# Performance work log

Hardware: AMD Instinct MI355X
Metric: run time of the kernel (lower is better)

Reference implementation:

```python
import jax, jax.numpy as jnp
import numpy as np

B, L, LATENT, HID, NTOK = 65536, 8, 256, 128, 5


def setup_inputs() -> dict:
    key = jax.random.key(0)
    ks = jax.random.split(key, 8)
    s = 0.05  # small init scale for stable GRU dynamics
    return {
        "latent_context": jax.random.normal(ks[0], (B, LATENT), jnp.float32),
        "target_sequence": jax.random.randint(ks[1], (B, L), 0, NTOK),
        "emb_table": jax.random.normal(ks[2], (NTOK + 1, HID), jnp.float32) * s,
        "W_ih": jax.random.normal(ks[3], (3 * LATENT, HID), jnp.float32) * s,
        "W_hh": jax.random.normal(ks[4], (3 * LATENT, LATENT), jnp.float32) * s,
        "b_ih": jnp.zeros((3 * LATENT,), jnp.float32),
        "b_hh": jnp.zeros((3 * LATENT,), jnp.float32),
        "W_out": jax.random.normal(ks[5], (NTOK, LATENT), jnp.float32) * s,
        "b_out": jnp.zeros((NTOK,), jnp.float32),
    }


def reference(latent_context, target_sequence, emb_table, W_ih, W_hh, b_ih, b_hh, W_out, b_out):
    b = latent_context.shape[0]
    start_idx = emb_table.shape[0] - 1  # start token index = num_tokens
    # Teacher forcing: input token at step 0 is <start>, then target[:, :-1]
    tokens = jnp.concatenate(
        [jnp.full((b, 1), start_idx, dtype=target_sequence.dtype), target_sequence[:, :-1]],
        axis=1,
    )  # (B, L)
    emb = emb_table[tokens]  # (B, L, HID) embedding gather, done once

    def gru_step(h, x):
        # x: (B, HID), h: (B, LATENT). PyTorch GRU cell math.
        gi = x @ W_ih.T + b_ih          # (B, 3*LATENT)
        gh = h @ W_hh.T + b_hh          # (B, 3*LATENT)
        i_r, i_z, i_n = jnp.split(gi, 3, axis=-1)
        h_r, h_z, h_n = jnp.split(gh, 3, axis=-1)
        r = jax.nn.sigmoid(i_r + h_r)
        z = jax.nn.sigmoid(i_z + h_z)
        n = jnp.tanh(i_n + r * h_n)
        h_new = (1.0 - z) * n + z * h
        step_logits = h_new @ W_out.T + b_out  # (B, NTOK)
        return h_new, step_logits

    _, logits = jax.lax.scan(gru_step, latent_context, jnp.swapaxes(emb, 0, 1))
    return jnp.swapaxes(logits, 0, 1)  # (B, L, NTOK)
```

## Files before the change

### kernel.cpp

```cpp
#include <hip/hip_runtime.h>
#include <hip/hip_bf16.h>


typedef __attribute__((ext_vector_type(8)))  __bf16 bf16x8;
typedef __attribute__((ext_vector_type(4)))  __bf16 bf16x4;
typedef __attribute__((ext_vector_type(16))) float  f32x16;

__device__ __forceinline__ float sigm(float x) {
    return __builtin_amdgcn_rcpf(1.f + __expf(-x));
}
__device__ __forceinline__ float tanh_fast(float x) {
    return __builtin_fmaf(2.f, __builtin_amdgcn_rcpf(1.f + __expf(-2.f * x)), -1.f);
}
__device__ __forceinline__ float f4get(const float4& v, int i) {
    return i == 0 ? v.x : i == 1 ? v.y : i == 2 ? v.z : v.w;
}

__global__ void k_gtable(const float* __restrict__ emb, const float* __restrict__ W_ih,
                         const float* __restrict__ b_ih, const float* __restrict__ b_hh,
                         float* __restrict__ G) {
    int tok = blockIdx.x;
    int j   = threadIdx.x;
    const float4* e4 = (const float4*)(emb + tok * 128);
    const float4* w4 = (const float4*)(W_ih + (size_t)j * 128);
    float s = 0.f;
#pragma unroll
    for (int k = 0; k < 32; ++k) {
        float4 a = e4[k], b = w4[k];
        s += a.x * b.x + a.y * b.y + a.z * b.z + a.w * b.w;
    }
    s += b_ih[j];
    if (j < 512) s += b_hh[j];
    G[tok * 768 + j] = s;
}

__global__ void k_wfrag(const float* __restrict__ Whh, __bf16* __restrict__ Wg) {
    int u = blockIdx.x * 256 + threadIdx.x;
    int lane = u & 63;
    int kc   = (u >> 6) & 15;
    int w    = (u >> 10) & 7;
    int g    = u >> 13;
    int row  = g * 256 + w * 32 + (lane & 31);
    int k0   = kc * 16 + (lane >> 5) * 8;
    const float* src = Whh + (size_t)row * 256 + k0;
    bf16x8 v;
#pragma unroll
    for (int j = 0; j < 8; ++j) v[j] = (__bf16)src[j];
    *(bf16x8*)(Wg + (size_t)u * 8) = v;
}

__global__ __launch_bounds__(512, 2) void k_main(
    const float* __restrict__ latent, const int* __restrict__ tgt,
    const float* __restrict__ Gtab, const __bf16* __restrict__ Wg,
    const float* __restrict__ b_hh, const float* __restrict__ Wout,
    const float* __restrict__ bout, float* __restrict__ out) {

    __shared__ __bf16 h_lds[2][2][16][64][8];
    __shared__ __bf16 woutf_lds[16][64][8];
    __shared__ int    tok_lds[64 * 9];
    __shared__ float  gtab_lds[6 * 772];
    __shared__ float  bhn_lds[256];
    __shared__ float  logit_lds[64 * 40];

    const int tid  = threadIdx.x;
    const int lane = tid & 63;
    const int w    = tid >> 6;
    const int hk   = lane >> 5;
    const int bn   = lane & 31;
    const int row0 = blockIdx.x * 64;

    const __bf16* wa = Wg + (size_t)w * 8192 + (size_t)lane * 8;

    {
        int b = tid >> 3, t = tid & 7;
        tok_lds[b * 9 + t] = (t == 0) ? 5 : tgt[(size_t)(row0 + b) * 8 + t - 1];
    }
    if (tid < 256) bhn_lds[tid] = b_hh[512 + tid];
#pragma unroll
    for (int tok = 0; tok < 6; ++tok)
        for (int i = tid; i < 768; i += 512) gtab_lds[tok * 772 + i] = Gtab[tok * 768 + i];
    for (int kc = w; kc < 16; kc += 8) {
        bf16x8 v;
        if (bn < 5) {
            const float* src = Wout + bn * 256 + kc * 16 + hk * 8;
#pragma unroll
            for (int j = 0; j < 8; ++j) v[j] = (__bf16)src[j];
        } else {
#pragma unroll
            for (int j = 0; j < 8; ++j) v[j] = (__bf16)0.f;
        }
        *(bf16x8*)&woutf_lds[kc][lane][0] = v;
    }
    const float bo0 = bout[0], bo1 = bout[1], bo2 = bout[2], bo3 = bout[3], bo4 = bout[4];

#pragma unroll
    for (int nt = 0; nt < 2; ++nt) {
        int grow = row0 + nt * 32 + bn;
#pragma unroll
        for (int q = 0; q < 4; ++q) {
            int cb = w * 32 + q * 8 + hk * 4;
            float4 hv = *(const float4*)(latent + (size_t)grow * 256 + cb);
            bf16x4 hb;
            hb[0] = (__bf16)hv.x; hb[1] = (__bf16)hv.y;
            hb[2] = (__bf16)hv.z; hb[3] = (__bf16)hv.w;
            *(bf16x4*)&h_lds[0][nt][2 * w + (q >> 1)][(q & 1) * 32 + bn][4 * hk] = hb;
        }
    }
    __syncthreads();

    for (int t = 0; t < 8; ++t) {
        const int cur = t & 1, nxt = cur ^ 1;
        f32x16 acc[3][2];
        {
            f32x16 zz;
#pragma unroll
            for (int i = 0; i < 16; ++i) zz[i] = 0.f;
#pragma unroll
            for (int g = 0; g < 3; ++g)
#pragma unroll
                for (int nt = 0; nt < 2; ++nt) acc[g][nt] = zz;
        }
#pragma unroll 4
        for (int kc = 0; kc < 16; ++kc) {
            bf16x8 a0 = *(const bf16x8*)(wa + kc * 512);
            bf16x8 a1 = *(const bf16x8*)(wa + 65536 + kc * 512);
            bf16x8 a2 = *(const bf16x8*)(wa + 131072 + kc * 512);
            bf16x8 b0 = *(const bf16x8*)&h_lds[cur][0][kc][lane][0];
            bf16x8 b1 = *(const bf16x8*)&h_lds[cur][1][kc][lane][0];
            acc[0][0] = __builtin_amdgcn_mfma_f32_32x32x16_bf16(a0, b0, acc[0][0], 0, 0, 0);
            acc[0][1] = __builtin_amdgcn_mfma_f32_32x32x16_bf16(a0, b1, acc[0][1], 0, 0, 0);
            acc[1][0] = __builtin_amdgcn_mfma_f32_32x32x16_bf16(a1, b0, acc[1][0], 0, 0, 0);
            acc[1][1] = __builtin_amdgcn_mfma_f32_32x32x16_bf16(a1, b1, acc[1][1], 0, 0, 0);
            acc[2][0] = __builtin_amdgcn_mfma_f32_32x32x16_bf16(a2, b0, acc[2][0], 0, 0, 0);
            acc[2][1] = __builtin_amdgcn_mfma_f32_32x32x16_bf16(a2, b1, acc[2][1], 0, 0, 0);
        }

        if ((w == 0 || w == 7) && t > 0) {
            const int nt = (w == 0) ? 0 : 1;
            f32x16 lacc;
#pragma unroll
            for (int i = 0; i < 16; ++i) lacc[i] = 0.f;
#pragma unroll 4
            for (int kc = 0; kc < 16; ++kc) {
                bf16x8 wf = *(const bf16x8*)&woutf_lds[kc][lane][0];
                bf16x8 bb = *(const bf16x8*)&h_lds[cur][nt][kc][lane][0];
                lacc = __builtin_amdgcn_mfma_f32_32x32x16_bf16(wf, bb, lacc, 0, 0, 0);
            }
            float* dst = &logit_lds[(nt * 32 + bn) * 40 + (t - 1) * 5];
            if (hk == 0) {
                dst[0] = lacc[0] + bo0; dst[1] = lacc[1] + bo1;
                dst[2] = lacc[2] + bo2; dst[3] = lacc[3] + bo3;
            } else {
                dst[4] = lacc[0] + bo4;
            }
        }

#pragma unroll
        for (int nt = 0; nt < 2; ++nt) {
            int tok = tok_lds[(nt * 32 + bn) * 9 + t];
            const float* Gt = gtab_lds + tok * 772;
#pragma unroll
            for (int q = 0; q < 4; ++q) {
                int cb = w * 32 + q * 8 + hk * 4;
                float4 g0 = *(const float4*)(Gt + cb);
                float4 g1 = *(const float4*)(Gt + 256 + cb);
                float4 g2 = *(const float4*)(Gt + 512 + cb);
                float4 bh = *(const float4*)&bhn_lds[cb];
                bf16x4 hold = *(const bf16x4*)&h_lds[cur][nt][2 * w + (q >> 1)][(q & 1) * 32 + bn][4 * hk];
                bf16x4 hb;
#pragma unroll
                for (int i = 0; i < 4; ++i) {
                    int r = 4 * q + i;
                    float ar = acc[0][nt][r] + f4get(g0, i);
                    float az = acc[1][nt][r] + f4get(g1, i);
                    float hn = acc[2][nt][r] + f4get(bh, i);
                    float rg = sigm(ar);
                    float zg = sigm(az);
                    float ng = tanh_fast(__builtin_fmaf(rg, hn, f4get(g2, i)));
                    float hvv = ng + zg * ((float)hold[i] - ng);
                    hb[i] = (__bf16)hvv;
                }
                *(bf16x4*)&h_lds[nxt][nt][2 * w + (q >> 1)][(q & 1) * 32 + bn][4 * hk] = hb;
            }
        }
        __syncthreads();
    }

    if (w == 0 || w == 7) {
        const int nt = (w == 0) ? 0 : 1;
        f32x16 lacc;
#pragma unroll
        for (int i = 0; i < 16; ++i) lacc[i] = 0.f;
#pragma unroll 4
        for (int kc = 0; kc < 16; ++kc) {
            bf16x8 wf = *(const bf16x8*)&woutf_lds[kc][lane][0];
            bf16x8 bb = *(const bf16x8*)&h_lds[0][nt][kc][lane][0];
            lacc = __builtin_amdgcn_mfma_f32_32x32x16_bf16(wf, bb, lacc, 0, 0, 0);
        }
        float* dst = &logit_lds[(nt * 32 + bn) * 40 + 7 * 5];
        if (hk == 0) {
            dst[0] = lacc[0] + bo0; dst[1] = lacc[1] + bo1;
            dst[2] = lacc[2] + bo2; dst[3] = lacc[3] + bo3;
        } else {
            dst[4] = lacc[0] + bo4;
        }
    }
    __syncthreads();
    for (int i = tid; i < 64 * 40; i += 512)
        out[(size_t)row0 * 40 + i] = logit_lds[i];
}

extern "C" void kernel_launch(void* const* d_in, const int* in_sizes, int n_in,
                              void* d_out, int out_size, void* d_ws, size_t ws_size,
                              hipStream_t stream) {
    const float* latent = (const float*)d_in[0];
    const int*   tgt    = (const int*)d_in[1];
    const float* emb    = (const float*)d_in[2];
    const float* W_ih   = (const float*)d_in[3];
    const float* W_hh   = (const float*)d_in[4];
    const float* b_ih   = (const float*)d_in[5];
    const float* b_hh   = (const float*)d_in[6];
    const float* W_out  = (const float*)d_in[7];
    const float* b_out  = (const float*)d_in[8];
    float* out = (float*)d_out;

    float*  Gtab = (float*)d_ws;
    __bf16* Wg   = (__bf16*)((char*)d_ws + 18432);

    k_gtable<<<6, 768, 0, stream>>>(emb, W_ih, b_ih, b_hh, Gtab);
    k_wfrag<<<96, 256, 0, stream>>>(W_hh, Wg);
    k_main<<<1024, 512, 0, stream>>>(latent, tgt, Gtab, Wg, b_hh, W_out, b_out, out);
}
```

Measured before the change: 298.5 us.

## Fold token gate table into MFMA via one-hot operands and prefetch weight fragments

The per-token input-gate contributions and the b_hn bias are packed as an extra K=16 fragment per gate. They are applied by multiplying one-hot token vectors through MFMA, which removes the gather of gate values from LDS and the scalar adds in the gate epilogue. A fourth accumulator holds the input n-gate term separately. The first two K-chunks of the W_hh fragments are kept in registers and reloaded across the step to hide global or L2 latency. __syncthreads is replaced by a raw barrier with an explicit lgkmcnt wait. This adds 8 extra MFMAs per step and more register pressure, and it also rounds the gate table to bf16.

```diff
diff --git a/kernel.cpp b/kernel.cpp
--- a/kernel.cpp
+++ b/kernel.cpp
@@ -12,8 +12,11 @@
 __device__ __forceinline__ float tanh_fast(float x) {
     return __builtin_fmaf(2.f, __builtin_amdgcn_rcpf(1.f + __expf(-2.f * x)), -1.f);
 }
-__device__ __forceinline__ float f4get(const float4& v, int i) {
-    return i == 0 ? v.x : i == 1 ? v.y : i == 2 ? v.z : v.w;
+__device__ __forceinline__ void lds_barrier() {
+    __builtin_amdgcn_sched_barrier(0);
+    asm volatile("s_waitcnt lgkmcnt(0)" ::: "memory");
+    __builtin_amdgcn_s_barrier();
+    __builtin_amdgcn_sched_barrier(0);
 }
 
 __global__ void k_gtable(const float* __restrict__ emb, const float* __restrict__ W_ih,
@@ -34,32 +37,49 @@
     G[tok * 768 + j] = s;
 }
 
-__global__ void k_wfrag(const float* __restrict__ Whh, __bf16* __restrict__ Wg) {
-    int u = blockIdx.x * 256 + threadIdx.x;
+__global__ void k_wfrag2(const float* __restrict__ Whh, const float* __restrict__ Gtab,
+                         const float* __restrict__ b_hh, __bf16* __restrict__ Wg) {
+    int u    = blockIdx.x * 256 + threadIdx.x;
     int lane = u & 63;
-    int kc   = (u >> 6) & 15;
-    int w    = (u >> 10) & 7;
-    int g    = u >> 13;
-    int row  = g * 256 + w * 32 + (lane & 31);
-    int k0   = kc * 16 + (lane >> 5) * 8;
-    const float* src = Whh + (size_t)row * 256 + k0;
+    int frag = u >> 6;
+    int w    = frag / 52;
+    int f    = frag - 52 * w;
+    int m    = w * 32 + (lane & 31);
+    int cb   = (lane >> 5) * 8;
     bf16x8 v;
-#pragma unroll
-    for (int j = 0; j < 8; ++j) v[j] = (__bf16)src[j];
+    if (f == 51) {
+#pragma unroll
+        for (int j = 0; j < 8; ++j) {
+            int c = cb + j;
+            v[j] = (c < 6) ? (__bf16)Gtab[c * 768 + 512 + m] : (__bf16)0.f;
+        }
+    } else {
+        int g = f / 17, kc = f - 17 * g;
+        if (kc < 16) {
+            const float* src = Whh + (size_t)(g * 256 + m) * 256 + kc * 16 + cb;
+#pragma unroll
+            for (int j = 0; j < 8; ++j) v[j] = (__bf16)src[j];
+        } else {
+#pragma unroll
+            for (int j = 0; j < 8; ++j) {
+                int c = cb + j;
+                float val = 0.f;
+                if (c < 6) val = (g < 2) ? Gtab[c * 768 + g * 256 + m] : b_hh[512 + m];
+                v[j] = (__bf16)val;
+            }
+        }
+    }
     *(bf16x8*)(Wg + (size_t)u * 8) = v;
 }
 
 __global__ __launch_bounds__(512, 2) void k_main(
     const float* __restrict__ latent, const int* __restrict__ tgt,
-    const float* __restrict__ Gtab, const __bf16* __restrict__ Wg,
-    const float* __restrict__ b_hh, const float* __restrict__ Wout,
+    const __bf16* __restrict__ Wg, const float* __restrict__ Wout,
     const float* __restrict__ bout, float* __restrict__ out) {
 
     __shared__ __bf16 h_lds[2][2][16][64][8];
+    __shared__ __bf16 onehot_lds[8][2][64][8];
     __shared__ __bf16 woutf_lds[16][64][8];
-    __shared__ int    tok_lds[64 * 9];
-    __shared__ float  gtab_lds[6 * 772];
-    __shared__ float  bhn_lds[256];
     __shared__ float  logit_lds[64 * 40];
 
     const int tid  = threadIdx.x;
@@ -69,16 +89,29 @@
     const int bn   = lane & 31;
     const int row0 = blockIdx.x * 64;
 
-    const __bf16* wa = Wg + (size_t)w * 8192 + (size_t)lane * 8;
-
-    {
-        int b = tid >> 3, t = tid & 7;
-        tok_lds[b * 9 + t] = (t == 0) ? 5 : tgt[(size_t)(row0 + b) * 8 + t - 1];
-    }
-    if (tid < 256) bhn_lds[tid] = b_hh[512 + tid];
-#pragma unroll
-    for (int tok = 0; tok < 6; ++tok)
-        for (int i = tid; i < 768; i += 512) gtab_lds[tok * 772 + i] = Gtab[tok * 768 + i];
+    const __bf16* wbase = Wg + ((size_t)(w * 52) * 64 + lane) * 8;
+
+    bf16x8 A16_0 = *(const bf16x8*)(wbase + 16 * 512);
+    bf16x8 A16_1 = *(const bf16x8*)(wbase + 33 * 512);
+    bf16x8 A16_2 = *(const bf16x8*)(wbase + 50 * 512);
+    bf16x8 A16_3 = *(const bf16x8*)(wbase + 51 * 512);
+    bf16x8 p0a = *(const bf16x8*)(wbase + 0 * 512);
+    bf16x8 p0b = *(const bf16x8*)(wbase + 17 * 512);
+    bf16x8 p0c = *(const bf16x8*)(wbase + 34 * 512);
+    bf16x8 p1a = *(const bf16x8*)(wbase + 1 * 512);
+    bf16x8 p1b = *(const bf16x8*)(wbase + 18 * 512);
+    bf16x8 p1c = *(const bf16x8*)(wbase + 35 * 512);
+
+    for (int r = tid; r < 1024; r += 512) {
+        int t = r >> 7, nt = (r >> 6) & 1, ln = r & 63;
+        int brow = row0 + nt * 32 + (ln & 31);
+        int tok = (t == 0) ? 5 : tgt[(size_t)brow * 8 + t - 1];
+        int cbase = (ln >> 5) * 8;
+        bf16x8 v;
+#pragma unroll
+        for (int j = 0; j < 8; ++j) v[j] = (__bf16)((cbase + j == tok) ? 1.f : 0.f);
+        *(bf16x8*)&onehot_lds[t][nt][ln][0] = v;
+    }
     for (int kc = w; kc < 16; kc += 8) {
         bf16x8 v;
         if (bn < 5) {
@@ -110,21 +143,51 @@
 
     for (int t = 0; t < 8; ++t) {
         const int cur = t & 1, nxt = cur ^ 1;
-        f32x16 acc[3][2];
+        f32x16 acc[4][2];
         {
             f32x16 zz;
 #pragma unroll
             for (int i = 0; i < 16; ++i) zz[i] = 0.f;
 #pragma unroll
-            for (int g = 0; g < 3; ++g)
+            for (int g = 0; g < 4; ++g)
 #pragma unroll
                 for (int nt = 0; nt < 2; ++nt) acc[g][nt] = zz;
         }
-#pragma unroll 4
-        for (int kc = 0; kc < 16; ++kc) {
-            bf16x8 a0 = *(const bf16x8*)(wa + kc * 512);
-            bf16x8 a1 = *(const bf16x8*)(wa + 65536 + kc * 512);
-            bf16x8 a2 = *(const bf16x8*)(wa + 131072 + kc * 512);
+        {
+            bf16x8 oh0 = *(const bf16x8*)&onehot_lds[t][0][lane][0];
+            bf16x8 oh1 = *(const bf16x8*)&onehot_lds[t][1][lane][0];
+            acc[0][0] = __builtin_amdgcn_mfma_f32_32x32x16_bf16(A16_0, oh0, acc[0][0], 0, 0, 0);
+            acc[0][1] = __builtin_amdgcn_mfma_f32_32x32x16_bf16(A16_0, oh1, acc[0][1], 0, 0, 0);
+            acc[1][0] = __builtin_amdgcn_mfma_f32_32x32x16_bf16(A16_1, oh0, acc[1][0], 0, 0, 0);
+            acc[1][1] = __builtin_amdgcn_mfma_f32_32x32x16_bf16(A16_1, oh1, acc[1][1], 0, 0, 0);
+            acc[2][0] = __builtin_amdgcn_mfma_f32_32x32x16_bf16(A16_2, oh0, acc[2][0], 0, 0, 0);
+            acc[2][1] = __builtin_amdgcn_mfma_f32_32x32x16_bf16(A16_2, oh1, acc[2][1], 0, 0, 0);
+            acc[3][0] = __builtin_amdgcn_mfma_f32_32x32x16_bf16(A16_3, oh0, acc[3][0], 0, 0, 0);
+            acc[3][1] = __builtin_amdgcn_mfma_f32_32x32x16_bf16(A16_3, oh1, acc[3][1], 0, 0, 0);
+        }
+        {
+            bf16x8 b0 = *(const bf16x8*)&h_lds[cur][0][0][lane][0];
+            bf16x8 b1 = *(const bf16x8*)&h_lds[cur][1][0][lane][0];
+            acc[0][0] = __builtin_amdgcn_mfma_f32_32x32x16_bf16(p0a, b0, acc[0][0], 0, 0, 0);
+            acc[0][1] = __builtin_amdgcn_mfma_f32_32x32x16_bf16(p0a, b1, acc[0][1], 0, 0, 0);
+            acc[1][0] = __builtin_amdgcn_mfma_f32_32x32x16_bf16(p0b, b0, acc[1][0], 0, 0, 0);
+            acc[1][1] = __builtin_amdgcn_mfma_f32_32x32x16_bf16(p0b, b1, acc[1][1], 0, 0, 0);
+            acc[2][0] = __builtin_amdgcn_mfma_f32_32x32x16_bf16(p0c, b0, acc[2][0], 0, 0, 0);
+            acc[2][1] = __builtin_amdgcn_mfma_f32_32x32x16_bf16(p0c, b1, acc[2][1], 0, 0, 0);
+            b0 = *(const bf16x8*)&h_lds[cur][0][1][lane][0];
+            b1 = *(const bf16x8*)&h_lds[cur][1][1][lane][0];
+            acc[0][0] = __builtin_amdgcn_mfma_f32_32x32x16_bf16(p1a, b0, acc[0][0], 0, 0, 0);
+            acc[0][1] = __builtin_amdgcn_mfma_f32_32x32x16_bf16(p1a, b1, acc[0][1], 0, 0, 0);
+            acc[1][0] = __builtin_amdgcn_mfma_f32_32x32x16_bf16(p1b, b0, acc[1][0], 0, 0, 0);
+            acc[1][1] = __builtin_amdgcn_mfma_f32_32x32x16_bf16(p1b, b1, acc[1][1], 0, 0, 0);
+            acc[2][0] = __builtin_amdgcn_mfma_f32_32x32x16_bf16(p1c, b0, acc[2][0], 0, 0, 0);
+            acc[2][1] = __builtin_amdgcn_mfma_f32_32x32x16_bf16(p1c, b1, acc[2][1], 0, 0, 0);
+        }
+#pragma unroll 2
+        for (int kc = 2; kc < 16; ++kc) {
+            bf16x8 a0 = *(const bf16x8*)(wbase + kc * 512);
+            bf16x8 a1 = *(const bf16x8*)(wbase + (17 + kc) * 512);
+            bf16x8 a2 = *(const bf16x8*)(wbase + (34 + kc) * 512);
             bf16x8 b0 = *(const bf16x8*)&h_lds[cur][0][kc][lane][0];
             bf16x8 b1 = *(const bf16x8*)&h_lds[cur][1][kc][lane][0];
             acc[0][0] = __builtin_amdgcn_mfma_f32_32x32x16_bf16(a0, b0, acc[0][0], 0, 0, 0);
@@ -134,6 +197,12 @@
             acc[2][0] = __builtin_amdgcn_mfma_f32_32x32x16_bf16(a2, b0, acc[2][0], 0, 0, 0);
             acc[2][1] = __builtin_amdgcn_mfma_f32_32x32x16_bf16(a2, b1, acc[2][1], 0, 0, 0);
         }
+        p0a = *(const bf16x8*)(wbase + 0 * 512);
+        p0b = *(const bf16x8*)(wbase + 17 * 512);
+        p0c = *(const bf16x8*)(wbase + 34 * 512);
+        p1a = *(const bf16x8*)(wbase + 1 * 512);
+        p1b = *(const bf16x8*)(wbase + 18 * 512);
+        p1c = *(const bf16x8*)(wbase + 35 * 512);
 
         if ((w == 0 || w == 7) && t > 0) {
             const int nt = (w == 0) ? 0 : 1;
@@ -157,33 +226,23 @@
 
 #pragma unroll
         for (int nt = 0; nt < 2; ++nt) {
-            int tok = tok_lds[(nt * 32 + bn) * 9 + t];
-            const float* Gt = gtab_lds + tok * 772;
 #pragma unroll
             for (int q = 0; q < 4; ++q) {
-                int cb = w * 32 + q * 8 + hk * 4;
-                float4 g0 = *(const float4*)(Gt + cb);
-                float4 g1 = *(const float4*)(Gt + 256 + cb);
-                float4 g2 = *(const float4*)(Gt + 512 + cb);
-                float4 bh = *(const float4*)&bhn_lds[cb];
                 bf16x4 hold = *(const bf16x4*)&h_lds[cur][nt][2 * w + (q >> 1)][(q & 1) * 32 + bn][4 * hk];
                 bf16x4 hb;
 #pragma unroll
                 for (int i = 0; i < 4; ++i) {
                     int r = 4 * q + i;
-                    float ar = acc[0][nt][r] + f4get(g0, i);
-                    float az = acc[1][nt][r] + f4get(g1, i);
-                    float hn = acc[2][nt][r] + f4get(bh, i);
-                    float rg = sigm(ar);
-                    float zg = sigm(az);
-                    float ng = tanh_fast(__builtin_fmaf(rg, hn, f4get(g2, i)));
-                    float hvv = ng + zg * ((float)hold[i] - ng);
-                    hb[i] = (__bf16)hvv;
+                    float rg = sigm(acc[0][nt][r]);
+                    float zg = sigm(acc[1][nt][r]);
+                    float ng = tanh_fast(__builtin_fmaf(rg, acc[2][nt][r], acc[3][nt][r]));
+                    float hv = ng + zg * ((float)hold[i] - ng);
+                    hb[i] = (__bf16)hv;
                 }
                 *(bf16x4*)&h_lds[nxt][nt][2 * w + (q >> 1)][(q & 1) * 32 + bn][4 * hk] = hb;
             }
         }
-        __syncthreads();
+        lds_barrier();
     }
 
     if (w == 0 || w == 7) {
@@ -225,9 +284,9 @@
     float* out = (float*)d_out;
 
     float*  Gtab = (float*)d_ws;
-    __bf16* Wg   = (__bf16*)((char*)d_ws + 18432);
+    __bf16* Wg2  = (__bf16*)((char*)d_ws + 18432);
 
     k_gtable<<<6, 768, 0, stream>>>(emb, W_ih, b_ih, b_hh, Gtab);
-    k_wfrag<<<96, 256, 0, stream>>>(W_hh, Wg);
-    k_main<<<1024, 512, 0, stream>>>(latent, tgt, Gtab, Wg, b_hh, W_out, b_out, out);
-}
+    k_wfrag2<<<104, 256, 0, stream>>>(W_hh, Gtab, b_hh, Wg2);
+    k_main<<<1024, 512, 0, stream>>>(latent, tgt, Wg2, W_out, b_out, out);
+}
```

Result: faster. 288.8 us (-3.3%).

## Fold token gate table into MFMA via one-hot and switch to 16x16x32 tiles

Applied to the files above, without the earlier changes.

Replaces the per-element gather of the precomputed input-gate table and the b_hh_n bias with an extra MFMA k-chunk that multiplies the weights by a one-hot token matrix held in LDS. This removes the gate-table and token LDS lookups from the elementwise stage and adds a fourth accumulator group so the n-gate input term stays separate. The main kernel moves to 16x16x32 bf16 MFMA with 16 waves (1024 threads) per block and a lighter LDS-only barrier, which changes per-wave register pressure and occupancy. The gate table and bias are now rounded to bf16 inside the MFMA, which adds some precision loss.

```diff
diff --git a/kernel.cpp b/kernel.cpp
--- a/kernel.cpp
+++ b/kernel.cpp
@@ -4,7 +4,7 @@
 
 typedef __attribute__((ext_vector_type(8)))  __bf16 bf16x8;
 typedef __attribute__((ext_vector_type(4)))  __bf16 bf16x4;
-typedef __attribute__((ext_vector_type(16))) float  f32x16;
+typedef __attribute__((ext_vector_type(4)))  float  f32x4;
 
 __device__ __forceinline__ float sigm(float x) {
     return __builtin_amdgcn_rcpf(1.f + __expf(-x));
@@ -12,8 +12,11 @@
 __device__ __forceinline__ float tanh_fast(float x) {
     return __builtin_fmaf(2.f, __builtin_amdgcn_rcpf(1.f + __expf(-2.f * x)), -1.f);
 }
-__device__ __forceinline__ float f4get(const float4& v, int i) {
-    return i == 0 ? v.x : i == 1 ? v.y : i == 2 ? v.z : v.w;
+__device__ __forceinline__ void lds_barrier() {
+    __builtin_amdgcn_sched_barrier(0);
+    asm volatile("s_waitcnt lgkmcnt(0)" ::: "memory");
+    __builtin_amdgcn_s_barrier();
+    __builtin_amdgcn_sched_barrier(0);
 }
 
 __global__ void k_gtable(const float* __restrict__ emb, const float* __restrict__ W_ih,
@@ -34,179 +37,185 @@
     G[tok * 768 + j] = s;
 }
 
-__global__ void k_wfrag(const float* __restrict__ Whh, __bf16* __restrict__ Wg) {
-    int u = blockIdx.x * 256 + threadIdx.x;
+__global__ void k_wfrag3(const float* __restrict__ Whh, const float* __restrict__ Gtab,
+                         const float* __restrict__ b_hh, __bf16* __restrict__ Wg) {
+    int u    = blockIdx.x * 256 + threadIdx.x;
     int lane = u & 63;
-    int kc   = (u >> 6) & 15;
-    int w    = (u >> 10) & 7;
-    int g    = u >> 13;
-    int row  = g * 256 + w * 32 + (lane & 31);
-    int k0   = kc * 16 + (lane >> 5) * 8;
-    const float* src = Whh + (size_t)row * 256 + k0;
+    int frag = u >> 6;
+    int w    = frag / 28;
+    int f    = frag - 28 * w;
+    int col  = w * 16 + (lane & 15);
+    int kq   = lane >> 4;
     bf16x8 v;
-#pragma unroll
-    for (int j = 0; j < 8; ++j) v[j] = (__bf16)src[j];
+    if (f < 24) {
+        int g = f >> 3, kc = f & 7;
+        const float* src = Whh + (size_t)(g * 256 + col) * 256 + kc * 32 + kq * 8;
+#pragma unroll
+        for (int j = 0; j < 8; ++j) v[j] = (__bf16)src[j];
+    } else {
+        int g = f - 24;
+#pragma unroll
+        for (int j = 0; j < 8; ++j) {
+            int k = kq * 8 + j;
+            float val = 0.f;
+            if (k < 6) {
+                val = (g == 0) ? Gtab[k * 768 + col]
+                    : (g == 1) ? Gtab[k * 768 + 256 + col]
+                    : (g == 2) ? b_hh[512 + col]
+                               : Gtab[k * 768 + 512 + col];
+            }
+            v[j] = (__bf16)val;
+        }
+    }
     *(bf16x8*)(Wg + (size_t)u * 8) = v;
 }
 
-__global__ __launch_bounds__(512, 2) void k_main(
+__global__ __launch_bounds__(1024) void k_main(
     const float* __restrict__ latent, const int* __restrict__ tgt,
-    const float* __restrict__ Gtab, const __bf16* __restrict__ Wg,
-    const float* __restrict__ b_hh, const float* __restrict__ Wout,
+    const __bf16* __restrict__ Wg, const float* __restrict__ Wout,
     const float* __restrict__ bout, float* __restrict__ out) {
 
-    __shared__ __bf16 h_lds[2][2][16][64][8];
-    __shared__ __bf16 woutf_lds[16][64][8];
-    __shared__ int    tok_lds[64 * 9];
-    __shared__ float  gtab_lds[6 * 772];
-    __shared__ float  bhn_lds[256];
+    __shared__ __bf16 h_lds[2][4][8][64][8];
+    __shared__ __bf16 onehot_lds[8][4][64][8];
+    __shared__ __bf16 woutf_lds[8][64][8];
     __shared__ float  logit_lds[64 * 40];
 
     const int tid  = threadIdx.x;
     const int lane = tid & 63;
     const int w    = tid >> 6;
-    const int hk   = lane >> 5;
-    const int bn   = lane & 31;
+    const int q    = lane >> 4;
+    const int n16  = lane & 15;
     const int row0 = blockIdx.x * 64;
 
-    const __bf16* wa = Wg + (size_t)w * 8192 + (size_t)lane * 8;
-
-    {
-        int b = tid >> 3, t = tid & 7;
-        tok_lds[b * 9 + t] = (t == 0) ? 5 : tgt[(size_t)(row0 + b) * 8 + t - 1];
-    }
-    if (tid < 256) bhn_lds[tid] = b_hh[512 + tid];
-#pragma unroll
-    for (int tok = 0; tok < 6; ++tok)
-        for (int i = tid; i < 768; i += 512) gtab_lds[tok * 772 + i] = Gtab[tok * 768 + i];
-    for (int kc = w; kc < 16; kc += 8) {
+    const __bf16* wbase = Wg + ((size_t)(w * 28) * 64 + lane) * 8;
+
+    const int kc_h  = w >> 1;
+    const int slotl = n16 + 16 * ((2 * w + (q >> 1)) & 3);
+    const int joff  = 4 * (q & 1);
+
+    if (tid < 512) {
+        int kc = tid >> 6, ln = tid & 63, m = ln & 15, kq2 = ln >> 4;
         bf16x8 v;
-        if (bn < 5) {
-            const float* src = Wout + bn * 256 + kc * 16 + hk * 8;
-#pragma unroll
-            for (int j = 0; j < 8; ++j) v[j] = (__bf16)src[j];
-        } else {
-#pragma unroll
-            for (int j = 0; j < 8; ++j) v[j] = (__bf16)0.f;
-        }
-        *(bf16x8*)&woutf_lds[kc][lane][0] = v;
-    }
+#pragma unroll
+        for (int j = 0; j < 8; ++j)
+            v[j] = (m < 5) ? (__bf16)Wout[m * 256 + kc * 32 + kq2 * 8 + j] : (__bf16)0.f;
+        *(bf16x8*)&woutf_lds[kc][ln][0] = v;
+    }
+    for (int s = tid; s < 2048; s += 1024) {
+        int t = s >> 8, nt = (s >> 6) & 3, ln = s & 63;
+        int nn = ln & 15, kq2 = ln >> 4;
+        int tok = (t == 0) ? 5 : tgt[(size_t)(row0 + nt * 16 + nn) * 8 + t - 1];
+        bf16x8 v;
+#pragma unroll
+        for (int j = 0; j < 8; ++j) v[j] = (__bf16)((kq2 * 8 + j == tok) ? 1.f : 0.f);
+        *(bf16x8*)&onehot_lds[t][nt][ln][0] = v;
+    }
+#pragma unroll
+    for (int nt = 0; nt < 4; ++nt) {
+        float4 hv = *(const float4*)(latent + (size_t)(row0 + nt * 16 + n16) * 256 + 16 * w + 4 * q);
+        bf16x4 hb;
+        hb[0] = (__bf16)hv.x; hb[1] = (__bf16)hv.y;
+        hb[2] = (__bf16)hv.z; hb[3] = (__bf16)hv.w;
+        *(bf16x4*)&h_lds[0][nt][kc_h][slotl][joff] = hb;
+    }
+    const int lw = (w == 0) ? 0 : (w == 5) ? 1 : (w == 10) ? 2 : (w == 15) ? 3 : -1;
     const float bo0 = bout[0], bo1 = bout[1], bo2 = bout[2], bo3 = bout[3], bo4 = bout[4];
-
-#pragma unroll
-    for (int nt = 0; nt < 2; ++nt) {
-        int grow = row0 + nt * 32 + bn;
-#pragma unroll
-        for (int q = 0; q < 4; ++q) {
-            int cb = w * 32 + q * 8 + hk * 4;
-            float4 hv = *(const float4*)(latent + (size_t)grow * 256 + cb);
-            bf16x4 hb;
-            hb[0] = (__bf16)hv.x; hb[1] = (__bf16)hv.y;
-            hb[2] = (__bf16)hv.z; hb[3] = (__bf16)hv.w;
-            *(bf16x4*)&h_lds[0][nt][2 * w + (q >> 1)][(q & 1) * 32 + bn][4 * hk] = hb;
-        }
-    }
     __syncthreads();
 
     for (int t = 0; t < 8; ++t) {
         const int cur = t & 1, nxt = cur ^ 1;
-        f32x16 acc[3][2];
+        f32x4 acc[4][4];
+#pragma unroll
+        for (int g = 0; g < 4; ++g)
+#pragma unroll
+            for (int nt = 0; nt < 4; ++nt)
+#pragma unroll
+                for (int i = 0; i < 4; ++i) acc[g][nt][i] = 0.f;
+
+#pragma unroll 2
+        for (int kc = 0; kc < 8; ++kc) {
+            bf16x8 a0 = *(const bf16x8*)(wbase + (size_t)kc * 512);
+            bf16x8 a1 = *(const bf16x8*)(wbase + (size_t)(8 + kc) * 512);
+            bf16x8 a2 = *(const bf16x8*)(wbase + (size_t)(16 + kc) * 512);
+#pragma unroll
+            for (int nt = 0; nt < 4; ++nt) {
+                bf16x8 bb = *(const bf16x8*)&h_lds[cur][nt][kc][lane][0];
+                acc[0][nt] = __builtin_amdgcn_mfma_f32_16x16x32_bf16(a0, bb, acc[0][nt], 0, 0, 0);
+                acc[1][nt] = __builtin_amdgcn_mfma_f32_16x16x32_bf16(a1, bb, acc[1][nt], 0, 0, 0);
+                acc[2][nt] = __builtin_amdgcn_mfma_f32_16x16x32_bf16(a2, bb, acc[2][nt], 0, 0, 0);
+            }
+        }
         {
-            f32x16 zz;
-#pragma unroll
-            for (int i = 0; i < 16; ++i) zz[i] = 0.f;
-#pragma unroll
-            for (int g = 0; g < 3; ++g)
-#pragma unroll
-                for (int nt = 0; nt < 2; ++nt) acc[g][nt] = zz;
-        }
-#pragma unroll 4
-        for (int kc = 0; kc < 16; ++kc) {
-            bf16x8 a0 = *(const bf16x8*)(wa + kc * 512);
-            bf16x8 a1 = *(const bf16x8*)(wa + 65536 + kc * 512);
-            bf16x8 a2 = *(const bf16x8*)(wa + 131072 + kc * 512);
-            bf16x8 b0 = *(const bf16x8*)&h_lds[cur][0][kc][lane][0];
-            bf16x8 b1 = *(const bf16x8*)&h_lds[cur][1][kc][lane][0];
-            acc[0][0] = __builtin_amdgcn_mfma_f32_32x32x16_bf16(a0, b0, acc[0][0], 0, 0, 0);
-            acc[0][1] = __builtin_amdgcn_mfma_f32_32x32x16_bf16(a0, b1, acc[0][1], 0, 0, 0);
-            acc[1][0] = __builtin_amdgcn_mfma_f32_32x32x16_bf16(a1, b0, acc[1][0], 0, 0, 0);
-            acc[1][1] = __builtin_amdgcn_mfma_f32_32x32x16_bf16(a1, b1, acc[1][1], 0, 0, 0);
-            acc[2][0] = __builtin_amdgcn_mfma_f32_32x32x16_bf16(a2, b0, acc[2][0], 0, 0, 0);
-            acc[2][1] = __builtin_amdgcn_mfma_f32_32x32x16_bf16(a2, b1, acc[2][1], 0, 0, 0);
-        }
-
-        if ((w == 0 || w == 7) && t > 0) {
-            const int nt = (w == 0) ? 0 : 1;
-            f32x16 lacc;
-#pragma unroll
-            for (int i = 0; i < 16; ++i) lacc[i] = 0.f;
-#pragma unroll 4
-            for (int kc = 0; kc < 16; ++kc) {
+            bf16x8 a0 = *(const bf16x8*)(wbase + (size_t)24 * 512);
+            bf16x8 a1 = *(const bf16x8*)(wbase + (size_t)25 * 512);
+            bf16x8 a2 = *(const bf16x8*)(wbase + (size_t)26 * 512);
+            bf16x8 a3 = *(const bf16x8*)(wbase + (size_t)27 * 512);
+#pragma unroll
+            for (int nt = 0; nt < 4; ++nt) {
+                bf16x8 oh = *(const bf16x8*)&onehot_lds[t][nt][lane][0];
+                acc[0][nt] = __builtin_amdgcn_mfma_f32_16x16x32_bf16(a0, oh, acc[0][nt], 0, 0, 0);
+                acc[1][nt] = __builtin_amdgcn_mfma_f32_16x16x32_bf16(a1, oh, acc[1][nt], 0, 0, 0);
+                acc[2][nt] = __builtin_amdgcn_mfma_f32_16x16x32_bf16(a2, oh, acc[2][nt], 0, 0, 0);
+                acc[3][nt] = __builtin_amdgcn_mfma_f32_16x16x32_bf16(a3, oh, acc[3][nt], 0, 0, 0);
+            }
+        }
+
+        if (lw >= 0 && t > 0) {
+            f32x4 lacc;
+#pragma unroll
+            for (int i = 0; i < 4; ++i) lacc[i] = 0.f;
+#pragma unroll
+            for (int kc = 0; kc < 8; ++kc) {
                 bf16x8 wf = *(const bf16x8*)&woutf_lds[kc][lane][0];
-                bf16x8 bb = *(const bf16x8*)&h_lds[cur][nt][kc][lane][0];
-                lacc = __builtin_amdgcn_mfma_f32_32x32x16_bf16(wf, bb, lacc, 0, 0, 0);
-            }
-            float* dst = &logit_lds[(nt * 32 + bn) * 40 + (t - 1) * 5];
-            if (hk == 0) {
+                bf16x8 bb = *(const bf16x8*)&h_lds[cur][lw][kc][lane][0];
+                lacc = __builtin_amdgcn_mfma_f32_16x16x32_bf16(wf, bb, lacc, 0, 0, 0);
+            }
+            float* dst = &logit_lds[(lw * 16 + n16) * 40 + (t - 1) * 5];
+            if (q == 0) {
                 dst[0] = lacc[0] + bo0; dst[1] = lacc[1] + bo1;
                 dst[2] = lacc[2] + bo2; dst[3] = lacc[3] + bo3;
-            } else {
+            } else if (q == 1) {
                 dst[4] = lacc[0] + bo4;
             }
         }
 
 #pragma unroll
-        for (int nt = 0; nt < 2; ++nt) {
-            int tok = tok_lds[(nt * 32 + bn) * 9 + t];
-            const float* Gt = gtab_lds + tok * 772;
-#pragma unroll
-            for (int q = 0; q < 4; ++q) {
-                int cb = w * 32 + q * 8 + hk * 4;
-                float4 g0 = *(const float4*)(Gt + cb);
-                float4 g1 = *(const float4*)(Gt + 256 + cb);
-                float4 g2 = *(const float4*)(Gt + 512 + cb);
-                float4 bh = *(const float4*)&bhn_lds[cb];
-                bf16x4 hold = *(const bf16x4*)&h_lds[cur][nt][2 * w + (q >> 1)][(q & 1) * 32 + bn][4 * hk];
-                bf16x4 hb;
-#pragma unroll
-                for (int i = 0; i < 4; ++i) {
-                    int r = 4 * q + i;
-                    float ar = acc[0][nt][r] + f4get(g0, i);
-                    float az = acc[1][nt][r] + f4get(g1, i);
-                    float hn = acc[2][nt][r] + f4get(bh, i);
-                    float rg = sigm(ar);
-                    float zg = sigm(az);
-                    float ng = tanh_fast(__builtin_fmaf(rg, hn, f4get(g2, i)));
-                    float hvv = ng + zg * ((float)hold[i] - ng);
-                    hb[i] = (__bf16)hvv;
-                }
-                *(bf16x4*)&h_lds[nxt][nt][2 * w + (q >> 1)][(q & 1) * 32 + bn][4 * hk] = hb;
-            }
-        }
-        __syncthreads();
-    }
-
-    if (w == 0 || w == 7) {
-        const int nt = (w == 0) ? 0 : 1;
-        f32x16 lacc;
-#pragma unroll
-        for (int i = 0; i < 16; ++i) lacc[i] = 0.f;
-#pragma unroll 4
-        for (int kc = 0; kc < 16; ++kc) {
+        for (int nt = 0; nt < 4; ++nt) {
+            bf16x4 hold = *(const bf16x4*)&h_lds[cur][nt][kc_h][slotl][joff];
+            bf16x4 hb;
+#pragma unroll
+            for (int i = 0; i < 4; ++i) {
+                float rg = sigm(acc[0][nt][i]);
+                float zg = sigm(acc[1][nt][i]);
+                float ng = tanh_fast(__builtin_fmaf(rg, acc[2][nt][i], acc[3][nt][i]));
+                float hv = ng + zg * ((float)hold[i] - ng);
+                hb[i] = (__bf16)hv;
+            }
+            *(bf16x4*)&h_lds[nxt][nt][kc_h][slotl][joff] = hb;
+        }
+        lds_barrier();
+    }
+
+    if (lw >= 0) {
+        f32x4 lacc;
+#pragma unroll
+        for (int i = 0; i < 4; ++i) lacc[i] = 0.f;
+#pragma unroll
+        for (int kc = 0; kc < 8; ++kc) {
             bf16x8 wf = *(const bf16x8*)&woutf_lds[kc][lane][0];
-            bf16x8 bb = *(const bf16x8*)&h_lds[0][nt][kc][lane][0];
-            lacc = __builtin_amdgcn_mfma_f32_32x32x16_bf16(wf, bb, lacc, 0, 0, 0);
-        }
-        float* dst = &logit_lds[(nt * 32 + bn) * 40 + 7 * 5];
-        if (hk == 0) {
+            bf16x8 bb = *(const bf16x8*)&h_lds[0][lw][kc][lane][0];
+            lacc = __builtin_amdgcn_mfma_f32_16x16x32_bf16(wf, bb, lacc, 0, 0, 0);
+        }
+        float* dst = &logit_lds[(lw * 16 + n16) * 40 + 7 * 5];
+        if (q == 0) {
             dst[0] = lacc[0] + bo0; dst[1] = lacc[1] + bo1;
             dst[2] = lacc[2] + bo2; dst[3] = lacc[3] + bo3;
-        } else {
+        } else if (q == 1) {
             dst[4] = lacc[0] + bo4;
         }
     }
     __syncthreads();
-    for (int i = tid; i < 64 * 40; i += 512)
+    for (int i = tid; i < 64 * 40; i += 1024)
         out[(size_t)row0 * 40 + i] = logit_lds[i];
 }
 
@@ -228,6 +237,6 @@
     __bf16* Wg   = (__bf16*)((char*)d_ws + 18432);
 
     k_gtable<<<6, 768, 0, stream>>>(emb, W_ih, b_ih, b_hh, Gtab);
-    k_wfrag<<<96, 256, 0, stream>>>(W_hh, Wg);
-    k_main<<<1024, 512, 0, stream>>>(latent, tgt, Gtab, Wg, b_hh, W_out, b_out, out);
-}
+    k_wfrag3<<<112, 256, 0, stream>>>(W_hh, Gtab, b_hh, Wg);
+    k_main<<<1024, 1024, 0, stream>>>(latent, tgt, Wg, W_out, b_out, out);
+}
```

After: 265.1 us. 11.2% less time.
